# Performance work log

Hardware: AMD Instinct MI355X
Metric: run time of the kernel (lower is better)

Reference implementation:

```python
import jax, jax.numpy as jnp
import numpy as np

B, T, C, R = 4, 2048, 2048, 256


def setup_inputs() -> dict:
    key = jax.random.key(0)
    ks = jax.random.split(key, 12)
    s = 0.02
    return {
        "x": jax.random.normal(ks[0], (B, T, C), dtype=jnp.float32),
        "h_state": jnp.zeros((B, C), dtype=jnp.float32),
        "ln_gamma": jnp.ones((C,), dtype=jnp.float32),
        "ln_beta": jnp.zeros((C,), dtype=jnp.float32),
        "wq_a": jax.random.normal(ks[1], (C, R), dtype=jnp.float32) * s,
        "wq_b": jax.random.normal(ks[2], (R, C), dtype=jnp.float32) * s,
        "wk_a": jax.random.normal(ks[3], (C, R), dtype=jnp.float32) * s,
        "wk_b": jax.random.normal(ks[4], (R, C), dtype=jnp.float32) * s,
        "wv_a": jax.random.normal(ks[5], (C, R), dtype=jnp.float32) * s,
        "wv_b": jax.random.normal(ks[6], (R, C), dtype=jnp.float32) * s,
        "out_w": jax.random.normal(ks[7], (C, C), dtype=jnp.float32) * s,
        "out_b": jnp.zeros((C,), dtype=jnp.float32),
        "time_decay": jnp.full((C,), -0.5, dtype=jnp.float32),
    }


def _layernorm(x, gamma, beta, eps=1e-5):
    mu = jnp.mean(x, axis=-1, keepdims=True)
    var = jnp.var(x, axis=-1, keepdims=True)
    return (x - mu) * jax.lax.rsqrt(var + eps) * gamma + beta


def reference(x, h_state, ln_gamma, ln_beta, wq_a, wq_b, wk_a, wk_b, wv_a, wv_b, out_w, out_b, time_decay):
    b, t, c = x.shape
    xn = _layernorm(x, ln_gamma, ln_beta)
    # token shift: mix current with previous token
    x_shift = jnp.concatenate([jnp.zeros((b, 1, c), xn.dtype), xn[:, :-1, :]], axis=1)
    mix = 0.5 * xn + 0.5 * x_shift
    # low-rank projections: (B,T,C) @ (C,R) @ (R,C)
    q = jnp.einsum('btc,cr,rd->btd', mix, wq_a, wq_b)
    k = jnp.einsum('btc,cr,rd->btd', mix, wk_a, wk_b)
    v = jnp.einsum('btc,cr,rd->btd', mix, wv_a, wv_b)
    decay = jnp.exp(-jnp.exp(time_decay))  # (C,)

    kv = (k * v).transpose(1, 0, 2)          # (T,B,C)
    sq = jax.nn.sigmoid(q).transpose(1, 0, 2)  # (T,B,C)

    def step(h, inp):
        kv_t, sq_t = inp
        h = decay * h + kv_t
        return h, sq_t * h

    h_final, ys = jax.lax.scan(step, h_state, (kv, sq))
    out = ys.transpose(1, 0, 2)               # (B,T,C)
    out = jnp.einsum('btc,dc->btd', out, out_w) + out_b
    return out, h_final
```

## Files before the change

### kernel.cpp

```cpp
#include <hip/hip_runtime.h>


typedef __attribute__((ext_vector_type(8))) __bf16 bf16x8;
typedef __attribute__((ext_vector_type(4))) float f32x4;

static constexpr int Bb = 4, Tt = 2048, Cc = 2048, Rr = 256;
static constexpr int Mrows = Bb * Tt;
static constexpr int NCH = 32, CLEN = 64;

__device__ __forceinline__ unsigned short f2bf(float f) {
  union { float f; unsigned u; } a; a.f = f;
  unsigned r = (a.u + 0x7FFFu + ((a.u >> 16) & 1u)) >> 16;
  return (unsigned short)r;
}
__device__ __forceinline__ float bf2f(unsigned short h) {
  union { unsigned u; float f; } a; a.u = ((unsigned)h) << 16;
  return a.f;
}

__device__ __forceinline__ void gload16(const void* g, void* l) {
  __builtin_amdgcn_global_load_lds(
      (const __attribute__((address_space(1))) void*)g,
      (__attribute__((address_space(3))) void*)l, 16, 0, 0);
}

__global__ void prep_weights(const float* __restrict__ wqa, const float* __restrict__ wka,
                             const float* __restrict__ wva, const float* __restrict__ wqb,
                             const float* __restrict__ wkb, const float* __restrict__ wvb,
                             const float* __restrict__ ow,  const float* __restrict__ td,
                             unsigned short* __restrict__ waT, unsigned short* __restrict__ wbT,
                             unsigned short* __restrict__ owT, float* __restrict__ decay,
                             float* __restrict__ decayL) {
  const int g = blockIdx.x * blockDim.x + threadIdx.x;
  const int stride = gridDim.x * blockDim.x;
  for (int i = g; i < 3 * Rr * Cc; i += stride) {
    int c = i & (Cc - 1); int jj = i >> 11; int p = jj >> 8; int r = jj & (Rr - 1);
    const float* w = (p == 0) ? wqa : ((p == 1) ? wka : wva);
    waT[i] = f2bf(w[(size_t)c * Rr + r]);
  }
  for (int i = g; i < 3 * Cc * Rr; i += stride) {
    int r = i & (Rr - 1); int d = (i >> 8) & (Cc - 1); int p = i >> 19;
    const float* w = (p == 0) ? wqb : ((p == 1) ? wkb : wvb);
    wbT[i] = f2bf(w[(size_t)r * Cc + d]);
  }
  for (int i = g; i < Cc * Cc; i += stride) owT[i] = f2bf(ow[i]);
  for (int i = g; i < Cc; i += stride) {
    float e = expf(td[i]);
    decay[i] = expf(-e);
    decayL[i] = expf(-(float)CLEN * e);
  }
}

__global__ __launch_bounds__(256) void lnmix_kernel(
    const float* __restrict__ x, const float* __restrict__ gamma,
    const float* __restrict__ beta, unsigned short* __restrict__ mix) {
  const int m = blockIdx.x;
  const int t = m & (Tt - 1);
  const float* xr = x + (size_t)m * Cc;
  float s0 = 0.f, q0 = 0.f, s1 = 0.f, q1 = 0.f;
  float4 cur[2], prv[2];
#pragma unroll
  for (int r = 0; r < 2; ++r) {
    int i = threadIdx.x + r * 256;
    float4 v = ((const float4*)xr)[i];
    cur[r] = v;
    s0 += v.x + v.y + v.z + v.w;
    q0 += v.x * v.x + v.y * v.y + v.z * v.z + v.w * v.w;
  }
  if (t > 0) {
    const float* xp = xr - Cc;
#pragma unroll
    for (int r = 0; r < 2; ++r) {
      int i = threadIdx.x + r * 256;
      float4 v = ((const float4*)xp)[i];
      prv[r] = v;
      s1 += v.x + v.y + v.z + v.w;
      q1 += v.x * v.x + v.y * v.y + v.z * v.z + v.w * v.w;
    }
  }
#pragma unroll
  for (int off = 32; off; off >>= 1) {
    s0 += __shfl_down(s0, off); q0 += __shfl_down(q0, off);
    s1 += __shfl_down(s1, off); q1 += __shfl_down(q1, off);
  }
  __shared__ float red[4][4];
  __shared__ float bc[4];
  if ((threadIdx.x & 63) == 0) {
    int w = threadIdx.x >> 6;
    red[w][0] = s0; red[w][1] = q0; red[w][2] = s1; red[w][3] = q1;
  }
  __syncthreads();
  if (threadIdx.x == 0) {
    float a0 = 0, b0 = 0, a1 = 0, b1 = 0;
    for (int w = 0; w < 4; ++w) { a0 += red[w][0]; b0 += red[w][1]; a1 += red[w][2]; b1 += red[w][3]; }
    float mu0 = a0 * (1.f / Cc);
    bc[0] = mu0; bc[1] = rsqrtf(b0 * (1.f / Cc) - mu0 * mu0 + 1e-5f);
    float mu1 = a1 * (1.f / Cc);
    bc[2] = mu1; bc[3] = rsqrtf(b1 * (1.f / Cc) - mu1 * mu1 + 1e-5f);
  }
  __syncthreads();
  const float mu0 = bc[0], rs0 = bc[1], mu1 = bc[2], rs1 = bc[3];
#pragma unroll
  for (int r = 0; r < 2; ++r) {
    int i = threadIdx.x + r * 256;
    float4 g = ((const float4*)gamma)[i];
    float4 bb = ((const float4*)beta)[i];
    float4 v = cur[r];
    float mx = (v.x - mu0) * rs0 * g.x + bb.x;
    float my = (v.y - mu0) * rs0 * g.y + bb.y;
    float mz = (v.z - mu0) * rs0 * g.z + bb.z;
    float mw = (v.w - mu0) * rs0 * g.w + bb.w;
    if (t > 0) {
      float4 u = prv[r];
      mx = 0.5f * (mx + (u.x - mu1) * rs1 * g.x + bb.x);
      my = 0.5f * (my + (u.y - mu1) * rs1 * g.y + bb.y);
      mz = 0.5f * (mz + (u.z - mu1) * rs1 * g.z + bb.z);
      mw = 0.5f * (mw + (u.w - mu1) * rs1 * g.w + bb.w);
    } else {
      mx *= 0.5f; my *= 0.5f; mz *= 0.5f; mw *= 0.5f;
    }
    ushort4 o;
    o.x = f2bf(mx); o.y = f2bf(my); o.z = f2bf(mz); o.w = f2bf(mw);
    ((ushort4*)mix)[(size_t)m * 512 + i] = o;
  }
}

template <bool STORE_BF16, bool ADD_BIAS>
__global__ __launch_bounds__(256, 2) void gemm_pipe(
    const unsigned short* __restrict__ A0p, long lda, long aStrideP,
    const unsigned short* __restrict__ B0p, long ldb, long bStrideP,
    void* c0, void* c1, void* c2, long ldc, int K,
    const float* __restrict__ bias, int nbx, int nby) {
  __shared__ unsigned short lds[3 * 12288];
  const int tid = threadIdx.x;
  const int nwg = gridDim.x;
  const int id = blockIdx.x;
  const int q = nwg >> 3;
  const int swz = (id & 7) * q + (id >> 3);
  const int per = nbx * nby;
  const int p = swz / per;
  const int r2 = swz - p * per;
  const int mblk = r2 / nbx;
  const int nblk = r2 - mblk * nbx;
  const unsigned short* A  = A0p + (long)p * aStrideP;
  const unsigned short* Bt = B0p + (long)p * bStrideP;
  void* Cout = (p == 0) ? c0 : (p == 1 ? c1 : c2);
  const long m0 = (long)mblk * 256, n0 = (long)nblk * 128;

  const int lane = tid & 63, wid = tid >> 6;
  const int wm = wid >> 1, wn = wid & 1;
  const int fr = lane & 15, fq = lane >> 4;

  const int srow = tid >> 2;
  const int s_src = (tid & 3) ^ ((tid >> 3) & 3);
  const unsigned short* Ag = A + (m0 + srow) * lda + s_src * 8;
  const unsigned short* Bg = Bt + (n0 + srow) * ldb + s_src * 8;

  const int swzs = fq ^ ((fr >> 1) & 3);
  const unsigned short* aBase = &lds[(wm * 128 + fr) * 32 + swzs * 8];
  const unsigned short* bBase = &lds[8192 + (wn * 64 + fr) * 32 + swzs * 8];

  f32x4 acc[8][4];
#pragma unroll
  for (int i = 0; i < 8; ++i)
#pragma unroll
    for (int j = 0; j < 4; ++j) acc[i][j] = (f32x4){0.f, 0.f, 0.f, 0.f};

  const int NT = K >> 5;

  auto stage = [&](int t, int buf) {
    unsigned short* dA = &lds[buf * 12288 + tid * 8];
    unsigned short* dB = &lds[buf * 12288 + 8192 + tid * 8];
    const long kt = (long)t * 32;
#pragma unroll
    for (int l = 0; l < 4; ++l)
      gload16(Ag + (long)(l * 64) * lda + kt, dA + l * 2048);
#pragma unroll
    for (int l = 0; l < 2; ++l)
      gload16(Bg + (long)(l * 64) * ldb + kt, dB + l * 2048);
  };

  stage(0, 0); stage(1, 1);
  int bufR = 0, bufS = 2;

  for (int t = 0; t < NT; ++t) {
    if (t < NT - 1) asm volatile("s_waitcnt vmcnt(6)" ::: "memory");
    else            asm volatile("s_waitcnt vmcnt(0)" ::: "memory");
    __builtin_amdgcn_s_barrier();
    __builtin_amdgcn_sched_barrier(0);

    const unsigned short* ab = aBase + bufR * 12288;
    const unsigned short* bb = bBase + bufR * 12288;

    bf16x8 bf[4], af[8];
#pragma unroll
    for (int j = 0; j < 4; ++j) bf[j] = *(const bf16x8*)(bb + j * 512);
#pragma unroll
    for (int i = 0; i < 8; ++i) af[i] = *(const bf16x8*)(ab + i * 512);
    if (t + 2 < NT) stage(t + 2, bufS);
    __builtin_amdgcn_s_setprio(1);
#pragma unroll
    for (int i = 0; i < 8; ++i)
#pragma unroll
      for (int j = 0; j < 4; ++j)
        acc[i][j] = __builtin_amdgcn_mfma_f32_16x16x32_bf16(af[i], bf[j], acc[i][j], 0, 0, 0);
    __builtin_amdgcn_s_setprio(0);

    bufR = (bufR == 2) ? 0 : bufR + 1;
    bufS = (bufS == 2) ? 0 : bufS + 1;
  }

#pragma unroll
  for (int j = 0; j < 4; ++j) {
    const long col = n0 + wn * 64 + j * 16 + fr;
    const float bv = ADD_BIAS ? bias[col] : 0.0f;
#pragma unroll
    for (int i = 0; i < 8; ++i) {
      const long row0 = m0 + wm * 128 + i * 16 + fq * 4;
#pragma unroll
      for (int r = 0; r < 4; ++r) {
        float val = acc[i][j][r] + bv;
        if (STORE_BF16)
          ((unsigned short*)Cout)[(row0 + r) * ldc + col] = f2bf(val);
        else
          ((float*)Cout)[(row0 + r) * ldc + col] = val;
      }
    }
  }
}

__global__ void addcvt_kernel(const float* __restrict__ p0, const float* __restrict__ p1,
                              unsigned short* __restrict__ o, int n4) {
  for (int i = blockIdx.x * blockDim.x + threadIdx.x; i < n4; i += gridDim.x * blockDim.x) {
    float4 a = ((const float4*)p0)[i];
    float4 b = ((const float4*)p1)[i];
    ushort4 r;
    r.x = f2bf(a.x + b.x); r.y = f2bf(a.y + b.y);
    r.z = f2bf(a.z + b.z); r.w = f2bf(a.w + b.w);
    ((ushort4*)o)[i] = r;
  }
}

__global__ void scan_phaseA(const unsigned short* __restrict__ k, const unsigned short* __restrict__ v,
                            const float* __restrict__ decay, float* __restrict__ hend) {
  const int g = blockIdx.x * 256 + threadIdx.x;
  const int c = g & (Cc - 1);
  const int j = (g >> 11) & (NCH - 1);
  const int b = g >> 16;
  const float d = decay[c];
  size_t base = ((size_t)(b * Tt + j * CLEN)) * Cc + c;
  float h = 0.f;
#pragma unroll 8
  for (int s = 0; s < CLEN; ++s) {
    size_t idx = base + (size_t)s * Cc;
    float kv = bf2f(k[idx]) * bf2f(v[idx]);
    h = fmaf(d, h, kv);
  }
  hend[(size_t)(b * NCH + j) * Cc + c] = h;
}

__global__ void scan_combine(const float* __restrict__ hend, const float* __restrict__ h0,
                             const float* __restrict__ decayL, float* __restrict__ Hin,
                             float* __restrict__ hfinal) {
  const int g = blockIdx.x * 256 + threadIdx.x;
  const int c = g & (Cc - 1);
  float H = h0[g];
  const float dl = decayL[c];
  const int b = g >> 11;
  for (int j = 0; j < NCH; ++j) {
    size_t idx = (size_t)(b * NCH + j) * Cc + c;
    Hin[idx] = H;
    H = fmaf(dl, H, hend[idx]);
  }
  hfinal[g] = H;
}

__global__ void scan_phaseB(const unsigned short* __restrict__ q, const unsigned short* __restrict__ k,
                            const unsigned short* __restrict__ v, const float* __restrict__ decay,
                            const float* __restrict__ Hin, unsigned short* __restrict__ ys) {
  const int g = blockIdx.x * 256 + threadIdx.x;
  const int c = g & (Cc - 1);
  const int j = (g >> 11) & (NCH - 1);
  const int b = g >> 16;
  const float d = decay[c];
  float h = Hin[(size_t)(b * NCH + j) * Cc + c];
  size_t base = ((size_t)(b * Tt + j * CLEN)) * Cc + c;
#pragma unroll 4
  for (int s = 0; s < CLEN; ++s) {
    size_t idx = base + (size_t)s * Cc;
    float kv = bf2f(k[idx]) * bf2f(v[idx]);
    h = fmaf(d, h, kv);
    float qq = bf2f(q[idx]);
    float sg = 1.f / (1.f + expf(-qq));
    ys[idx] = f2bf(sg * h);
  }
}

extern "C" void kernel_launch(void* const* d_in, const int* in_sizes, int n_in,
                              void* d_out, int out_size, void* d_ws, size_t ws_size,
                              hipStream_t stream) {
  const float* x   = (const float*)d_in[0];
  const float* h0  = (const float*)d_in[1];
  const float* gam = (const float*)d_in[2];
  const float* bet = (const float*)d_in[3];
  const float* wqa = (const float*)d_in[4];
  const float* wqb = (const float*)d_in[5];
  const float* wka = (const float*)d_in[6];
  const float* wkb = (const float*)d_in[7];
  const float* wva = (const float*)d_in[8];
  const float* wvb = (const float*)d_in[9];
  const float* ow  = (const float*)d_in[10];
  const float* ob  = (const float*)d_in[11];
  const float* td  = (const float*)d_in[12];
  float* out = (float*)d_out;

  char* ws = (char*)d_ws;
  unsigned short* waT   = (unsigned short*)(ws + 0);
  unsigned short* wbT   = (unsigned short*)(ws + 3145728);
  unsigned short* owT   = (unsigned short*)(ws + 6291456);
  float*          decay = (float*)(ws + 14680064);
  float*          decayL= (float*)(ws + 14688256);
  unsigned short* mixb  = (unsigned short*)(ws + 14761984);
  unsigned short* tmp   = (unsigned short*)(ws + 48316416);
  unsigned short* vp    = (unsigned short*)(ws + 60899328);
  float*          hend  = (float*)(ws + 94453760);
  float*          Hin   = (float*)(ws + 95502336);
  float* P0 = (float*)d_out;
  float* P1 = P0 + (size_t)Mrows * 768;
  unsigned short* qp = (unsigned short*)d_out;
  unsigned short* kp = qp + (size_t)Mrows * Cc;
  float* hfinal = out + (size_t)Mrows * Cc;
  unsigned short* ysb = mixb;

  prep_weights<<<1024, 256, 0, stream>>>(wqa, wka, wva, wqb, wkb, wvb, ow, td,
                                         waT, wbT, owT, decay, decayL);
  lnmix_kernel<<<Mrows, 256, 0, stream>>>(x, gam, bet, mixb);

  gemm_pipe<false, false><<<384, 256, 0, stream>>>(
      mixb, Cc, 1024, waT, Cc, 1024,
      P0, P1, nullptr, 768, 1024, nullptr, 6, 32);
  addcvt_kernel<<<1024, 256, 0, stream>>>(P0, P1, tmp, Mrows * 768 / 4);

  gemm_pipe<true, false><<<1536, 256, 0, stream>>>(
      tmp, 768, 256, wbT, Rr, (long)Cc * Rr,
      qp, kp, vp, Cc, Rr, nullptr, 16, 32);

  scan_phaseA<<<(Bb * NCH * Cc) / 256, 256, 0, stream>>>(kp, vp, decay, hend);
  scan_combine<<<(Bb * Cc) / 256, 256, 0, stream>>>(hend, h0, decayL, Hin, hfinal);
  scan_phaseB<<<(Bb * NCH * Cc) / 256, 256, 0, stream>>>(qp, kp, vp, decay, Hin, ysb);

  gemm_pipe<false, true><<<512, 256, 0, stream>>>(
      ysb, Cc, 0, owT, Cc, 0,
      out, out, out, Cc, Cc, ob, 16, 32);
}
```

Before: 244.5 us.

## Loop over q/k/v problems inside one GEMM block to pipeline across outputs

The GEMM kernel gains a multi-problem mode in which each workgroup processes several independent GEMM problems (q, k, v second-stage projections) back to back. The LDS prefetch pipeline keeps running across problem boundaries, and each accumulator tile is written out when its K loop finishes. The second-stage GEMM now launches 512 blocks that each handle three problems instead of 1536 blocks handling one. This removes the per-block pipeline fill and drain for the short K=256 GEMMs, at the cost of fewer resident blocks and epilogue stores that now sit inside the main loop.

```diff
diff --git a/kernel.cpp b/kernel.cpp
--- a/kernel.cpp
+++ b/kernel.cpp
@@ -126,10 +126,10 @@
 }
 
 template <bool STORE_BF16, bool ADD_BIAS>
-__global__ __launch_bounds__(256, 2) void gemm_pipe(
-    const unsigned short* __restrict__ A0p, long lda, long aStrideP,
-    const unsigned short* __restrict__ B0p, long ldb, long bStrideP,
-    void* c0, void* c1, void* c2, long ldc, int K,
+__global__ __launch_bounds__(256, 2) void gemm_mp(
+    const unsigned short* __restrict__ A0, long lda, long aStrideP,
+    const unsigned short* __restrict__ B0, long ldb, long bStrideP,
+    void* c0, void* c1, void* c2, long ldc, int NT2, int npLoop,
     const float* __restrict__ bias, int nbx, int nby) {
   __shared__ unsigned short lds[3 * 12288];
   const int tid = threadIdx.x;
@@ -138,13 +138,11 @@
   const int q = nwg >> 3;
   const int swz = (id & 7) * q + (id >> 3);
   const int per = nbx * nby;
-  const int p = swz / per;
-  const int r2 = swz - p * per;
+  const int pgrid = swz / per;
+  const int r2 = swz - pgrid * per;
   const int mblk = r2 / nbx;
   const int nblk = r2 - mblk * nbx;
-  const unsigned short* A  = A0p + (long)p * aStrideP;
-  const unsigned short* Bt = B0p + (long)p * bStrideP;
-  void* Cout = (p == 0) ? c0 : (p == 1 ? c1 : c2);
+  const int pgBase = pgrid * npLoop;
   const long m0 = (long)mblk * 256, n0 = (long)nblk * 128;
 
   const int lane = tid & 63, wid = tid >> 6;
@@ -153,8 +151,8 @@
 
   const int srow = tid >> 2;
   const int s_src = (tid & 3) ^ ((tid >> 3) & 3);
-  const unsigned short* Ag = A + (m0 + srow) * lda + s_src * 8;
-  const unsigned short* Bg = Bt + (n0 + srow) * ldb + s_src * 8;
+  const unsigned short* Ag = A0 + (long)pgBase * aStrideP + (m0 + srow) * lda + s_src * 8;
+  const unsigned short* Bg = B0 + (long)pgBase * bStrideP + (n0 + srow) * ldb + s_src * 8;
 
   const int swzs = fq ^ ((fr >> 1) & 3);
   const unsigned short* aBase = &lds[(wm * 128 + fr) * 32 + swzs * 8];
@@ -166,12 +164,12 @@
 #pragma unroll
     for (int j = 0; j < 4; ++j) acc[i][j] = (f32x4){0.f, 0.f, 0.f, 0.f};
 
-  const int NT = K >> 5;
-
-  auto stage = [&](int t, int buf) {
+  const int TT = NT2 * npLoop;
+
+  auto stage = [&](int kIn, int buf) {
     unsigned short* dA = &lds[buf * 12288 + tid * 8];
     unsigned short* dB = &lds[buf * 12288 + 8192 + tid * 8];
-    const long kt = (long)t * 32;
+    const long kt = (long)kIn * 32;
 #pragma unroll
     for (int l = 0; l < 4; ++l)
       gload16(Ag + (long)(l * 64) * lda + kt, dA + l * 2048);
@@ -180,11 +178,34 @@
       gload16(Bg + (long)(l * 64) * ldb + kt, dB + l * 2048);
   };
 
+  auto writeC = [&](int pe) {
+    void* Cp = (pe == 0) ? c0 : (pe == 1 ? c1 : c2);
+#pragma unroll
+    for (int j = 0; j < 4; ++j) {
+      const long col = n0 + wn * 64 + j * 16 + fr;
+      const float bv = ADD_BIAS ? bias[col] : 0.0f;
+#pragma unroll
+      for (int i = 0; i < 8; ++i) {
+        const long row0 = m0 + wm * 128 + i * 16 + fq * 4;
+#pragma unroll
+        for (int r = 0; r < 4; ++r) {
+          float val = acc[i][j][r] + bv;
+          if (STORE_BF16)
+            ((unsigned short*)Cp)[(row0 + r) * ldc + col] = f2bf(val);
+          else
+            ((float*)Cp)[(row0 + r) * ldc + col] = val;
+        }
+      }
+    }
+  };
+
   stage(0, 0); stage(1, 1);
+  int sk = 2;
   int bufR = 0, bufS = 2;
-
-  for (int t = 0; t < NT; ++t) {
-    if (t < NT - 1) asm volatile("s_waitcnt vmcnt(6)" ::: "memory");
+  int rk = 0, rp = 0;
+
+  for (int t = 0; t < TT; ++t) {
+    if (t < TT - 1) asm volatile("s_waitcnt vmcnt(6)" ::: "memory");
     else            asm volatile("s_waitcnt vmcnt(0)" ::: "memory");
     __builtin_amdgcn_s_barrier();
     __builtin_amdgcn_sched_barrier(0);
@@ -197,7 +218,10 @@
     for (int j = 0; j < 4; ++j) bf[j] = *(const bf16x8*)(bb + j * 512);
 #pragma unroll
     for (int i = 0; i < 8; ++i) af[i] = *(const bf16x8*)(ab + i * 512);
-    if (t + 2 < NT) stage(t + 2, bufS);
+    if (t + 2 < TT) {
+      stage(sk, bufS);
+      if (++sk == NT2) { sk = 0; Ag += aStrideP; Bg += bStrideP; }
+    }
     __builtin_amdgcn_s_setprio(1);
 #pragma unroll
     for (int i = 0; i < 8; ++i)
@@ -206,26 +230,20 @@
         acc[i][j] = __builtin_amdgcn_mfma_f32_16x16x32_bf16(af[i], bf[j], acc[i][j], 0, 0, 0);
     __builtin_amdgcn_s_setprio(0);
 
+    if (++rk == NT2) {
+      rk = 0;
+      writeC(pgBase + rp);
+      ++rp;
+      if (rp < npLoop) {
+#pragma unroll
+        for (int i = 0; i < 8; ++i)
+#pragma unroll
+          for (int j = 0; j < 4; ++j) acc[i][j] = (f32x4){0.f, 0.f, 0.f, 0.f};
+      }
+    }
+
     bufR = (bufR == 2) ? 0 : bufR + 1;
     bufS = (bufS == 2) ? 0 : bufS + 1;
-  }
-
-#pragma unroll
-  for (int j = 0; j < 4; ++j) {
-    const long col = n0 + wn * 64 + j * 16 + fr;
-    const float bv = ADD_BIAS ? bias[col] : 0.0f;
-#pragma unroll
-    for (int i = 0; i < 8; ++i) {
-      const long row0 = m0 + wm * 128 + i * 16 + fq * 4;
-#pragma unroll
-      for (int r = 0; r < 4; ++r) {
-        float val = acc[i][j][r] + bv;
-        if (STORE_BF16)
-          ((unsigned short*)Cout)[(row0 + r) * ldc + col] = f2bf(val);
-        else
-          ((float*)Cout)[(row0 + r) * ldc + col] = val;
-      }
-    }
   }
 }
 
@@ -336,20 +354,20 @@
                                          waT, wbT, owT, decay, decayL);
   lnmix_kernel<<<Mrows, 256, 0, stream>>>(x, gam, bet, mixb);
 
-  gemm_pipe<false, false><<<384, 256, 0, stream>>>(
+  gemm_mp<false, false><<<384, 256, 0, stream>>>(
       mixb, Cc, 1024, waT, Cc, 1024,
-      P0, P1, nullptr, 768, 1024, nullptr, 6, 32);
+      P0, P1, nullptr, 768, 32, 1, nullptr, 6, 32);
   addcvt_kernel<<<1024, 256, 0, stream>>>(P0, P1, tmp, Mrows * 768 / 4);
 
-  gemm_pipe<true, false><<<1536, 256, 0, stream>>>(
+  gemm_mp<true, false><<<512, 256, 0, stream>>>(
       tmp, 768, 256, wbT, Rr, (long)Cc * Rr,
-      qp, kp, vp, Cc, Rr, nullptr, 16, 32);
+      qp, kp, vp, Cc, 8, 3, nullptr, 16, 32);
 
   scan_phaseA<<<(Bb * NCH * Cc) / 256, 256, 0, stream>>>(kp, vp, decay, hend);
   scan_combine<<<(Bb * Cc) / 256, 256, 0, stream>>>(hend, h0, decayL, Hin, hfinal);
   scan_phaseB<<<(Bb * NCH * Cc) / 256, 256, 0, stream>>>(qp, kp, vp, decay, Hin, ysb);
 
-  gemm_pipe<false, true><<<512, 256, 0, stream>>>(
+  gemm_mp<false, true><<<512, 256, 0, stream>>>(
       ysb, Cc, 0, owT, Cc, 0,
-      out, out, out, Cc, Cc, ob, 16, 32);
-}
+      out, out, out, Cc, 64, 1, ob, 16, 32);
+}
```

Result: slower. 255.7 us (+4.6%).

## Replace second low-rank GEMM with LDS-resident A tile and fragment-packed B weights

Applied to the files above, without the earlier changes.

The generic pipelined GEMM for the rank-256 up-projection is replaced by a dedicated kernel. Each 512-thread block loads its whole 256x256 bf16 A slab into LDS once, using an XOR swizzle, and then sweeps four 128-column N tiles. B weights are pre-packed in prep_weights into the exact MFMA fragment order, so each lane reads them straight from global memory with contiguous 16-byte loads. This is meant to remove repeated A reloads and B staging through LDS, at the cost of 128KB of LDS per block (one block per CU) and no overlap between the load phase and compute.

```diff
diff --git a/kernel.cpp b/kernel.cpp
--- a/kernel.cpp
+++ b/kernel.cpp
@@ -28,7 +28,7 @@
                              const float* __restrict__ wva, const float* __restrict__ wqb,
                              const float* __restrict__ wkb, const float* __restrict__ wvb,
                              const float* __restrict__ ow,  const float* __restrict__ td,
-                             unsigned short* __restrict__ waT, unsigned short* __restrict__ wbT,
+                             unsigned short* __restrict__ waT, unsigned short* __restrict__ wbP,
                              unsigned short* __restrict__ owT, float* __restrict__ decay,
                              float* __restrict__ decayL) {
   const int g = blockIdx.x * blockDim.x + threadIdx.x;
@@ -39,9 +39,16 @@
     waT[i] = f2bf(w[(size_t)c * Rr + r]);
   }
   for (int i = g; i < 3 * Cc * Rr; i += stride) {
-    int r = i & (Rr - 1); int d = (i >> 8) & (Cc - 1); int p = i >> 19;
+    int e = i & 7;
+    int l = (i >> 3) & 63;
+    int j = (i >> 9) & 3;
+    int kt = (i >> 11) & 7;
+    int n64 = (i >> 14) & 31;
+    int p = i >> 19;
     const float* w = (p == 0) ? wqb : ((p == 1) ? wkb : wvb);
-    wbT[i] = f2bf(w[(size_t)r * Cc + d]);
+    int r = kt * 32 + ((l >> 4) << 3) + e;
+    int d = n64 * 64 + j * 16 + (l & 15);
+    wbP[i] = f2bf(w[(size_t)r * Cc + d]);
   }
   for (int i = g; i < Cc * Cc; i += stride) owT[i] = f2bf(ow[i]);
   for (int i = g; i < Cc; i += stride) {
@@ -229,6 +236,84 @@
   }
 }
 
+__global__ __launch_bounds__(512, 1) void gemm_g2(
+    const unsigned short* __restrict__ tmp, const unsigned short* __restrict__ wbP,
+    unsigned short* __restrict__ qo, unsigned short* __restrict__ ko,
+    unsigned short* __restrict__ vo) {
+  __shared__ unsigned short Al[65536];
+  const int tid = threadIdx.x;
+  const int nwg = gridDim.x;
+  const int id0 = blockIdx.x;
+  const int qq = nwg >> 3;
+  const int id = (id0 & 7) * qq + (id0 >> 3);
+  const int mblk = id / 12;
+  const int rem = id - mblk * 12;
+  const int p = rem >> 2;
+  const int nbg = rem & 3;
+
+  {
+    const int rowb = tid >> 5;
+    const int slot = tid & 31;
+    const int s_src = slot ^ (rowb & 7);
+    const unsigned short* src = tmp + ((size_t)(mblk * 256 + rowb)) * 768 + p * 256 + s_src * 8;
+    unsigned short* dst = &Al[(size_t)tid * 8];
+#pragma unroll
+    for (int c = 0; c < 16; ++c)
+      gload16(src + (size_t)c * 16 * 768, dst + c * 4096);
+  }
+  asm volatile("s_waitcnt vmcnt(0)" ::: "memory");
+  __builtin_amdgcn_s_barrier();
+
+  const int lane = tid & 63, wid = tid >> 6;
+  const int wm = wid >> 1, wn = wid & 1;
+  const int fr = lane & 15, fq = lane >> 4;
+
+  unsigned short* Cout = (p == 0) ? qo : (p == 1 ? ko : vo);
+
+  for (int s = 0; s < 4; ++s) {
+    const int nbCol = nbg * 512 + s * 128;
+    const int n64 = (nbCol >> 6) + wn;
+    const unsigned short* bbase = wbP + ((size_t)(p * 32 + n64) * 8) * 2048 + lane * 8;
+
+    f32x4 acc[4][4];
+#pragma unroll
+    for (int i = 0; i < 4; ++i)
+#pragma unroll
+      for (int j = 0; j < 4; ++j) acc[i][j] = (f32x4){0.f, 0.f, 0.f, 0.f};
+
+#pragma unroll
+    for (int kt = 0; kt < 8; ++kt) {
+      bf16x8 af[4], bf[4];
+#pragma unroll
+      for (int j = 0; j < 4; ++j)
+        bf[j] = *(const bf16x8*)(bbase + kt * 2048 + j * 512);
+#pragma unroll
+      for (int i = 0; i < 4; ++i) {
+        const int row = wm * 64 + i * 16 + fr;
+        const int sl = (kt * 4 + fq) ^ (fr & 7);
+        af[i] = *(const bf16x8*)&Al[row * 256 + sl * 8];
+      }
+#pragma unroll
+      for (int i = 0; i < 4; ++i)
+#pragma unroll
+        for (int j = 0; j < 4; ++j)
+          acc[i][j] = __builtin_amdgcn_mfma_f32_16x16x32_bf16(af[i], bf[j], acc[i][j], 0, 0, 0);
+    }
+
+#pragma unroll
+    for (int j = 0; j < 4; ++j) {
+      const long col = nbCol + wn * 64 + j * 16 + fr;
+#pragma unroll
+      for (int i = 0; i < 4; ++i) {
+        const long row0 = (long)mblk * 256 + wm * 64 + i * 16 + fq * 4;
+#pragma unroll
+        for (int r = 0; r < 4; ++r)
+          Cout[(row0 + r) * Cc + col] = f2bf(acc[i][j][r]);
+      }
+    }
+  }
+}
+
 __global__ void addcvt_kernel(const float* __restrict__ p0, const float* __restrict__ p1,
                               unsigned short* __restrict__ o, int n4) {
   for (int i = blockIdx.x * blockDim.x + threadIdx.x; i < n4; i += gridDim.x * blockDim.x) {
@@ -316,7 +401,7 @@
 
   char* ws = (char*)d_ws;
   unsigned short* waT   = (unsigned short*)(ws + 0);
-  unsigned short* wbT   = (unsigned short*)(ws + 3145728);
+  unsigned short* wbP   = (unsigned short*)(ws + 3145728);
   unsigned short* owT   = (unsigned short*)(ws + 6291456);
   float*          decay = (float*)(ws + 14680064);
   float*          decayL= (float*)(ws + 14688256);
@@ -333,7 +418,7 @@
   unsigned short* ysb = mixb;
 
   prep_weights<<<1024, 256, 0, stream>>>(wqa, wka, wva, wqb, wkb, wvb, ow, td,
-                                         waT, wbT, owT, decay, decayL);
+                                         waT, wbP, owT, decay, decayL);
   lnmix_kernel<<<Mrows, 256, 0, stream>>>(x, gam, bet, mixb);
 
   gemm_pipe<false, false><<<384, 256, 0, stream>>>(
@@ -341,9 +426,7 @@
       P0, P1, nullptr, 768, 1024, nullptr, 6, 32);
   addcvt_kernel<<<1024, 256, 0, stream>>>(P0, P1, tmp, Mrows * 768 / 4);
 
-  gemm_pipe<true, false><<<1536, 256, 0, stream>>>(
-      tmp, 768, 256, wbT, Rr, (long)Cc * Rr,
-      qp, kp, vp, Cc, Rr, nullptr, 16, 32);
+  gemm_g2<<<384, 512, 0, stream>>>(tmp, wbP, qp, kp, vp);
 
   scan_phaseA<<<(Bb * NCH * Cc) / 256, 256, 0, stream>>>(kp, vp, decay, hend);
   scan_combine<<<(Bb * Cc) / 256, 256, 0, stream>>>(hend, h0, decayL, Hin, hfinal);
@@ -351,5 +434,5 @@
 
   gemm_pipe<false, true><<<512, 256, 0, stream>>>(
       ysb, Cc, 0, owT, Cc, 0,
-      out, out, out, Cc, Cc, ob, 16, 32);
-}
+      out, out, out, Cc, 2048, ob, 16, 32);
+}
```

Result: slower. 254.8 us (+4.2%).
